# Kernel optimization log

Hardware: AMD Instinct MI355X
Metric: run time of the kernel (lower is better)

## Reference

```python
import jax, jax.numpy as jnp
import numpy as np

N = 4096
NUM_FEATURES = 1870
HIDDEN = 256
EMBED = 16
ALPHA = 0.2
NEG_BIG = -9e15
EPS = 1e-12


def setup_inputs() -> dict:
    key = jax.random.key(0)
    ks = jax.random.split(key, 9)
    x = jax.random.normal(ks[0], (N, NUM_FEATURES), dtype=jnp.float32)
    # sparse-ish binary adjacency mask (avg degree ~ 41) with self loops
    adj = (jax.random.uniform(ks[1], (N, N)) < 0.01).astype(jnp.float32)
    adj = jnp.maximum(adj, jnp.eye(N, dtype=jnp.float32))
    M = jax.random.uniform(ks[2], (N, N), dtype=jnp.float32)
    s1 = 1.0 / np.sqrt(NUM_FEATURES)
    s2 = 1.0 / np.sqrt(HIDDEN)
    W1 = jax.random.normal(ks[3], (NUM_FEATURES, HIDDEN), dtype=jnp.float32) * s1
    a_self1 = jax.random.normal(ks[4], (HIDDEN, 1), dtype=jnp.float32) * s2
    a_neighs1 = jax.random.normal(ks[5], (HIDDEN, 1), dtype=jnp.float32) * s2
    W2 = jax.random.normal(ks[6], (HIDDEN, EMBED), dtype=jnp.float32) * s2
    a_self2 = jax.random.normal(ks[7], (EMBED, 1), dtype=jnp.float32) / np.sqrt(EMBED)
    a_neighs2 = jax.random.normal(ks[8], (EMBED, 1), dtype=jnp.float32) / np.sqrt(EMBED)
    return {"x": x, "adj": adj, "M": M, "W1": W1, "a_self1": a_self1,
            "a_neighs1": a_neighs1, "W2": W2, "a_self2": a_self2, "a_neighs2": a_neighs2}


def gat_layer(x, adj, M, W, a_self, a_neighs, alpha):
    h = x @ W                                  # [N, out]
    f_self = h @ a_self                        # [N, 1]
    f_neigh = h @ a_neighs                     # [N, 1]
    e = jax.nn.leaky_relu((f_self + f_neigh.T) * M, negative_slope=alpha)  # [N, N]
    e = jnp.where(adj > 0, e, NEG_BIG)
    att = jax.nn.softmax(e, axis=1)            # row-stochastic over neighbors
    return jax.nn.elu(att @ h)                 # [N, out]


def reference(x, adj, M, W1, a_self1, a_neighs1, W2, a_self2, a_neighs2):
    h = gat_layer(x, adj, M, W1, a_self1, a_neighs1, ALPHA)
    h = gat_layer(h, adj, M, W2, a_self2, a_neighs2, ALPHA)
    # F.normalize(h, p=2, dim=1): divide by max(norm, eps)
    norm = jnp.maximum(jnp.linalg.norm(h, axis=1, keepdims=True), EPS)
    z = h / norm                               # [N, EMBED]
    A_pred = jax.nn.sigmoid(z @ z.T)           # [N, N]
    return (A_pred, z)
```

## Files before the change

kernel.cpp:

```cpp
#include <hip/hip_runtime.h>
#include <math.h>

#define NN 4096
#define NFEAT 1870
#define KPAD 1920
#define HID 256
#define EMB 16
#define MAXDEG 128

typedef __attribute__((ext_vector_type(8))) _Float16 f16x8;
typedef __attribute__((ext_vector_type(4))) float f32x4;

__device__ __forceinline__ ushort f2h(float f) {
    _Float16 h = (_Float16)f;
    return __builtin_bit_cast(ushort, h);
}

__global__ __launch_bounds__(256) void xcv_kernel(
    const float* __restrict__ x, ushort* __restrict__ xf)
{
    const int idx = blockIdx.x * 256 + threadIdx.x;
    const int row = idx / 240;
    const int c0 = (idx % 240) * 8;
    float v[8];
    if (c0 + 8 <= NFEAT) {
#pragma unroll
        for (int j = 0; j < 4; ++j) {
            float2 t = *(const float2*)&x[(size_t)row * NFEAT + c0 + j * 2];
            v[j * 2] = t.x; v[j * 2 + 1] = t.y;
        }
    } else {
#pragma unroll
        for (int j = 0; j < 8; ++j)
            v[j] = (c0 + j < NFEAT) ? x[(size_t)row * NFEAT + c0 + j] : 0.f;
    }
    ushort u[8];
#pragma unroll
    for (int j = 0; j < 8; ++j) u[j] = f2h(v[j]);
    *(int4*)&xf[(size_t)row * KPAD + c0] = *(int4*)u;
}

__global__ __launch_bounds__(256) void conv_w1t_kernel(
    const float* __restrict__ W1, ushort* __restrict__ Wh)
{
    __shared__ float t[64][65];
    const int tid = threadIdx.x;
    const int k0 = blockIdx.x * 64, n0 = blockIdx.y * 64;
    const int kk = tid >> 2, c4 = (tid & 3) * 16;
#pragma unroll
    for (int j = 0; j < 4; ++j) {
        int k = k0 + kk;
        float4 v = make_float4(0.f, 0.f, 0.f, 0.f);
        if (k < NFEAT) v = *(const float4*)&W1[(size_t)k * HID + n0 + c4 + j * 4];
        t[kk][c4 + j * 4 + 0] = v.x; t[kk][c4 + j * 4 + 1] = v.y;
        t[kk][c4 + j * 4 + 2] = v.z; t[kk][c4 + j * 4 + 3] = v.w;
    }
    __syncthreads();
    const int on = tid >> 2, ok4 = (tid & 3) * 16;
#pragma unroll
    for (int j = 0; j < 4; ++j) {
        ushort hh[4];
#pragma unroll
        for (int i = 0; i < 4; ++i)
            hh[i] = f2h(t[ok4 + j * 4 + i][on]);
        size_t o = (size_t)(n0 + on) * KPAD + k0 + ok4 + j * 4;
        *(ushort4*)&Wh[o] = *(ushort4*)hh;
    }
}

__global__ __launch_bounds__(256) void gemm_xw1(
    const ushort* __restrict__ Ag,
    const ushort* __restrict__ Bg,
    float* __restrict__ Cpart)
{
    __shared__ ushort Ah[128 * 64];
    __shared__ ushort Bh[64 * 64];
    const int tid = threadIdx.x;
    const int lane = tid & 63;
    const int w = tid >> 6;
    const int wr = w >> 1, wc = w & 1;
    const int row0 = blockIdx.x * 128;
    const int col0 = blockIdx.y * 64;
    const int kbeg = blockIdx.z * 512;
    const int kend = min(KPAD, kbeg + 512);
    const int nsteps = (kend - kbeg) >> 6;

    const int fr = lane & 15, fs = lane >> 4;

    const int a_row = tid >> 1;
    const int a_sk0 = (tid & 1) * 4;
    const int b_row = tid >> 2;
    const int b_sk0 = (tid & 3) * 2;

    const size_t a_gbase = (size_t)(row0 + a_row) * KPAD;
    const size_t b_gbase = (size_t)(col0 + b_row) * KPAD;

    int4 ra[4], rb[2];
#define LOADAB(K0)                                                        \
    {                                                                     \
        _Pragma("unroll")                                                 \
        for (int i = 0; i < 4; ++i)                                       \
            ra[i] = *(const int4*)&Ag[a_gbase + (K0) + (a_sk0 + i) * 8];  \
        _Pragma("unroll")                                                 \
        for (int i = 0; i < 2; ++i)                                       \
            rb[i] = *(const int4*)&Bg[b_gbase + (K0) + (b_sk0 + i) * 8];  \
    }

    LOADAB(kbeg);
    f32x4 acc[4][2] = {};

    for (int ks = 0; ks < nsteps; ++ks) {
        __syncthreads();
#pragma unroll
        for (int i = 0; i < 4; ++i)
            *(int4*)&Ah[(a_row * 8 + ((a_sk0 + i) ^ (a_row & 7))) * 8] = ra[i];
#pragma unroll
        for (int i = 0; i < 2; ++i)
            *(int4*)&Bh[(b_row * 8 + ((b_sk0 + i) ^ (b_row & 7))) * 8] = rb[i];
        __syncthreads();
        if (ks + 1 < nsteps) LOADAB(kbeg + (ks + 1) * 64);

        f16x8 af[4][2], bf[2][2];
#pragma unroll
        for (int m = 0; m < 4; ++m) {
            int r = wr * 64 + m * 16 + fr;
#pragma unroll
            for (int kf = 0; kf < 2; ++kf) {
                int sk = kf * 4 + fs;
                af[m][kf] = *(const f16x8*)&Ah[(r * 8 + (sk ^ (r & 7))) * 8];
            }
        }
#pragma unroll
        for (int n = 0; n < 2; ++n) {
            int r = wc * 32 + n * 16 + fr;
#pragma unroll
            for (int kf = 0; kf < 2; ++kf) {
                int sk = kf * 4 + fs;
                bf[n][kf] = *(const f16x8*)&Bh[(r * 8 + (sk ^ (r & 7))) * 8];
            }
        }
#pragma unroll
        for (int m = 0; m < 4; ++m)
#pragma unroll
            for (int n = 0; n < 2; ++n)
#pragma unroll
                for (int kf = 0; kf < 2; ++kf)
                    acc[m][n] = __builtin_amdgcn_mfma_f32_16x16x32_f16(
                        af[m][kf], bf[n][kf], acc[m][n], 0, 0, 0);
    }
    float* Cp = Cpart + (size_t)blockIdx.z * NN * HID;
#pragma unroll
    for (int m = 0; m < 4; ++m)
#pragma unroll
        for (int n = 0; n < 2; ++n)
#pragma unroll
            for (int r = 0; r < 4; ++r) {
                int row = row0 + wr * 64 + m * 16 + fs * 4 + r;
                int col = col0 + wc * 32 + n * 16 + fr;
                Cp[(size_t)row * HID + col] = acc[m][n][r];
            }
}

__global__ __launch_bounds__(256) void reduce_h1f_kernel(
    const float* __restrict__ part, float* __restrict__ h1,
    const float* __restrict__ a_s, const float* __restrict__ a_n,
    float* __restrict__ fs, float* __restrict__ fn)
{
    const int tid = threadIdx.x, wv = tid >> 6, lane = tid & 63;
    const int row = blockIdx.x * 4 + wv;
    const int d0 = lane * 4;
    const size_t o = (size_t)row * HID + d0;
    float4 s = *(const float4*)&part[o];
#pragma unroll
    for (int ch = 1; ch < 4; ++ch) {
        float4 p = *(const float4*)&part[(size_t)ch * NN * HID + o];
        s.x += p.x; s.y += p.y; s.z += p.z; s.w += p.w;
    }
    *(float4*)&h1[o] = s;
    float4 as4 = *(const float4*)&a_s[d0];
    float4 an4 = *(const float4*)&a_n[d0];
    float ps = s.x * as4.x + s.y * as4.y + s.z * as4.z + s.w * as4.w;
    float pn = s.x * an4.x + s.y * an4.y + s.z * an4.z + s.w * an4.w;
#pragma unroll
    for (int off = 32; off > 0; off >>= 1) {
        ps += __shfl_down(ps, off, 64);
        pn += __shfl_down(pn, off, 64);
    }
    if (lane == 0) { fs[row] = ps; fn[row] = pn; }
}

__global__ __launch_bounds__(256) void extract_kernel(
    const float* __restrict__ adj, const float* __restrict__ Mmat,
    int* __restrict__ nnz, int* __restrict__ gidx, float* __restrict__ Mg)
{
    __shared__ int sidx[4][MAXDEG];
    const int tid = threadIdx.x;
    const int wv = tid >> 6, lane = tid & 63;
    const int row = blockIdx.x * 4 + wv;

    int base = 0;
#pragma unroll 4
    for (int t = 0; t < 16; ++t) {
        int j0 = t * 256 + lane * 4;
        float4 a = *(const float4*)&adj[(size_t)row * NN + j0];
        float av[4] = {a.x, a.y, a.z, a.w};
#pragma unroll
        for (int c = 0; c < 4; ++c) {
            unsigned long long mb = __ballot(av[c] > 0.f);
            if (av[c] > 0.f) {
                int pos = base + (int)__popcll(mb & ((1ull << lane) - 1ull));
                if (pos < MAXDEG) sidx[wv][pos] = j0 + c;
            }
            base += (int)__popcll(mb);
        }
    }
    const int cnt = min(base, MAXDEG);
    if (lane == 0) nnz[row] = cnt;
    for (int s = lane; s < cnt; s += 64) {
        int j = sidx[wv][s];
        gidx[(size_t)row * MAXDEG + s] = j;
        Mg[(size_t)row * MAXDEG + s] = Mmat[(size_t)row * NN + j];
    }
}

__global__ __launch_bounds__(256) void spmm1_kernel(
    const int* __restrict__ nnz, const int* __restrict__ gidx,
    const float* __restrict__ Mg,
    const float* __restrict__ fs, const float* __restrict__ fn,
    const float* __restrict__ h1, float* __restrict__ g1)
{
    __shared__ float p_s[MAXDEG];
    __shared__ int j_s[MAXDEG];
    __shared__ float wred[4], wsum[4];
    const int row = blockIdx.x;
    const int tid = threadIdx.x;
    const int lane = tid & 63, wv = tid >> 6;
    const int cnt = nnz[row];
    const float fsi = fs[row];

    float lmax = -3.0e38f;
    for (int s = tid; s < cnt; s += 256) {
        int j = gidx[(size_t)row * MAXDEG + s];
        j_s[s] = j;
        float e = (fsi + fn[j]) * Mg[(size_t)row * MAXDEG + s];
        e = (e > 0.f) ? e : 0.2f * e;
        p_s[s] = e;
        lmax = fmaxf(lmax, e);
    }
#pragma unroll
    for (int off = 32; off > 0; off >>= 1)
        lmax = fmaxf(lmax, __shfl_down(lmax, off, 64));
    if (lane == 0) wred[wv] = lmax;
    __syncthreads();
    const float m = fmaxf(fmaxf(wred[0], wred[1]), fmaxf(wred[2], wred[3]));

    float lsum = 0.f;
    for (int s = tid; s < cnt; s += 256) {
        float p = __expf(p_s[s] - m);
        p_s[s] = p;
        lsum += p;
    }
#pragma unroll
    for (int off = 32; off > 0; off >>= 1)
        lsum += __shfl_down(lsum, off, 64);
    if (lane == 0) wsum[wv] = lsum;
    __syncthreads();
    const float inv = 1.f / (wsum[0] + wsum[1] + wsum[2] + wsum[3]);

    float acc = 0.f;
#pragma unroll 4
    for (int s = 0; s < cnt; ++s)
        acc += p_s[s] * h1[(size_t)j_s[s] * HID + tid];
    float v = acc * inv;
    v = (v > 0.f) ? v : (__expf(v) - 1.f);
    g1[(size_t)row * HID + tid] = v;
}

__global__ __launch_bounds__(256) void gemm_h2_kernel(
    const float* __restrict__ g1, const float* __restrict__ W2,
    const float* __restrict__ a_s2, const float* __restrict__ a_n2,
    float* __restrict__ h2, float* __restrict__ fs2, float* __restrict__ fn2)
{
    __shared__ float Ws[256][16];
    __shared__ float Gs[16][257];
    const int tid = threadIdx.x;
    const int row0 = blockIdx.x * 16;
#pragma unroll
    for (int i = 0; i < 16; ++i) {
        int idx = tid + i * 256;
        Ws[idx >> 4][idx & 15] = W2[idx];
    }
#pragma unroll
    for (int i = 0; i < 16; ++i) {
        int idx = tid + i * 256;
        Gs[idx >> 8][idx & 255] = g1[(size_t)(row0 + (idx >> 8)) * HID + (idx & 255)];
    }
    __syncthreads();
    const int r = tid >> 4, c = tid & 15;
    float acc = 0.f;
#pragma unroll 8
    for (int k = 0; k < 256; ++k)
        acc += Gs[r][k] * Ws[k][c];
    h2[(size_t)(row0 + r) * EMB + c] = acc;

    float ps = acc * a_s2[c];
    float pn = acc * a_n2[c];
#pragma unroll
    for (int off = 1; off < 16; off <<= 1) {
        ps += __shfl_xor(ps, off, 64);
        pn += __shfl_xor(pn, off, 64);
    }
    if (c == 0) { fs2[row0 + r] = ps; fn2[row0 + r] = pn; }
}

__global__ __launch_bounds__(256) void spmm2_kernel(
    const int* __restrict__ nnz, const int* __restrict__ gidx,
    const float* __restrict__ Mg,
    const float* __restrict__ fs, const float* __restrict__ fn,
    const float* __restrict__ h2, float* __restrict__ z)
{
    __shared__ float p_s[4][MAXDEG];
    __shared__ int j_s[4][MAXDEG];
    const int tid = threadIdx.x;
    const int wv = tid >> 6, lane = tid & 63;
    const int row = blockIdx.x * 4 + wv;
    const int cnt = nnz[row];
    const float fsi = fs[row];

    float lmax = -3.0e38f;
    for (int s = lane; s < cnt; s += 64) {
        int j = gidx[(size_t)row * MAXDEG + s];
        j_s[wv][s] = j;
        float e = (fsi + fn[j]) * Mg[(size_t)row * MAXDEG + s];
        e = (e > 0.f) ? e : 0.2f * e;
        p_s[wv][s] = e;
        lmax = fmaxf(lmax, e);
    }
#pragma unroll
    for (int off = 1; off < 64; off <<= 1)
        lmax = fmaxf(lmax, __shfl_xor(lmax, off, 64));

    float lsum = 0.f;
    for (int s = lane; s < cnt; s += 64) {
        float p = __expf(p_s[wv][s] - lmax);
        p_s[wv][s] = p;
        lsum += p;
    }
#pragma unroll
    for (int off = 1; off < 64; off <<= 1)
        lsum += __shfl_xor(lsum, off, 64);
    const float inv = 1.f / lsum;

    const int s0 = lane >> 4, d = lane & 15;
    float acc = 0.f;
    for (int s = s0; s < cnt; s += 4)
        acc += p_s[wv][s] * h2[(size_t)j_s[wv][s] * EMB + d];
    acc += __shfl_xor(acc, 16, 64);
    acc += __shfl_xor(acc, 32, 64);

    float v = acc * inv;
    v = (v > 0.f) ? v : (__expf(v) - 1.f);
    float ss = v * v;
#pragma unroll
    for (int off = 1; off < 16; off <<= 1)
        ss += __shfl_xor(ss, off, 64);
    float zn = v / fmaxf(sqrtf(ss), 1e-12f);
    if (lane < 16) z[(size_t)row * EMB + lane] = zn;
}

__global__ __launch_bounds__(256) void apred_kernel(
    const float* __restrict__ z, float* __restrict__ out)
{
    __shared__ float zr[64][20];
    __shared__ float zc[64][20];
    const int tid = threadIdx.x;
    const int r0 = blockIdx.y * 64, c0 = blockIdx.x * 64;
#pragma unroll
    for (int i = 0; i < 4; ++i) {
        int idx = tid + i * 256;
        int rr = idx >> 4, d = idx & 15;
        zr[rr][d] = z[(size_t)(r0 + rr) * EMB + d];
        zc[rr][d] = z[(size_t)(c0 + rr) * EMB + d];
    }
    __syncthreads();
    const int tx = tid & 15, ty = tid >> 4;
    float rb[4][16], cb[4][16];
#pragma unroll
    for (int i = 0; i < 4; ++i)
#pragma unroll
        for (int d = 0; d < 16; ++d) {
            rb[i][d] = zr[ty * 4 + i][d];
            cb[i][d] = zc[tx * 4 + i][d];
        }
#pragma unroll
    for (int i = 0; i < 4; ++i) {
        float4 o;
        float v[4];
#pragma unroll
        for (int j = 0; j < 4; ++j) {
            float s = 0.f;
#pragma unroll
            for (int d = 0; d < 16; ++d) s += rb[i][d] * cb[j][d];
            v[j] = 1.f / (1.f + __expf(-s));
        }
        o.x = v[0]; o.y = v[1]; o.z = v[2]; o.w = v[3];
        *reinterpret_cast<float4*>(
            &out[(size_t)(r0 + ty * 4 + i) * NN + c0 + tx * 4]) = o;
    }
}

extern "C" void kernel_launch(void* const* d_in, const int* in_sizes, int n_in,
                              void* d_out, int out_size, void* d_ws, size_t ws_size,
                              hipStream_t stream)
{
    const float* x    = (const float*)d_in[0];
    const float* adj  = (const float*)d_in[1];
    const float* Mm   = (const float*)d_in[2];
    const float* W1   = (const float*)d_in[3];
    const float* a_s1 = (const float*)d_in[4];
    const float* a_n1 = (const float*)d_in[5];
    const float* W2   = (const float*)d_in[6];
    const float* a_s2 = (const float*)d_in[7];
    const float* a_n2 = (const float*)d_in[8];

    float* out = (float*)d_out;
    float* z   = out + (size_t)NN * NN;

    char* w = (char*)d_ws;
    float* part  = (float*)w;  w += (size_t)4 * NN * HID * 4;
    float* h1    = (float*)w;  w += (size_t)NN * HID * 4;
    float* g1    = (float*)w;  w += (size_t)NN * HID * 4;
    ushort* xf16 = (ushort*)w; w += (size_t)NN * KPAD * 2;
    ushort* W1Th = (ushort*)w; w += (size_t)HID * KPAD * 2;
    float* h2    = (float*)w;  w += (size_t)NN * EMB * 4;
    int*   nnzp  = (int*)w;    w += NN * 4;
    int*   gidx  = (int*)w;    w += (size_t)NN * MAXDEG * 4;
    float* Mg    = (float*)w;  w += (size_t)NN * MAXDEG * 4;
    float* fs1   = (float*)w;  w += NN * 4;
    float* fn1   = (float*)w;  w += NN * 4;
    float* fs2   = (float*)w;  w += NN * 4;
    float* fn2   = (float*)w;  w += NN * 4;

    xcv_kernel<<<NN * 240 / 256, 256, 0, stream>>>(x, xf16);
    conv_w1t_kernel<<<dim3(30, 4), 256, 0, stream>>>(W1, W1Th);
    extract_kernel<<<NN / 4, 256, 0, stream>>>(adj, Mm, nnzp, gidx, Mg);

    gemm_xw1<<<dim3(32, 4, 4), 256, 0, stream>>>(xf16, W1Th, part);
    reduce_h1f_kernel<<<NN / 4, 256, 0, stream>>>(part, h1, a_s1, a_n1, fs1, fn1);
    spmm1_kernel<<<NN, 256, 0, stream>>>(nnzp, gidx, Mg, fs1, fn1, h1, g1);

    gemm_h2_kernel<<<256, 256, 0, stream>>>(g1, W2, a_s2, a_n2, h2, fs2, fn2);
    spmm2_kernel<<<NN / 4, 256, 0, stream>>>(nnzp, gidx, Mg, fs2, fn2, h2, z);

    apred_kernel<<<dim3(64, 64), 256, 0, stream>>>(z, out);
}
```

Before: 117.7 us.

## Fuse prep kernels, use LDS-free split-K GEMM, stage partials in output buffer

Merges the x conversion, W1 transpose and adjacency extraction into one launch with block-range dispatch. The X·W1 GEMM drops LDS staging and barriers: each wave loads MFMA fragments straight from global memory. K is padded to 2048 and split 8 ways into 256-wide chunks on a 1D grid. Split-K partials now go into the A_pred output region, which apred_kernel overwrites later, so the workspace is smaller. The risks are more uncoalesced global fragment loads and double the partial-sum traffic in the reduce step.

Result: faster. 109.4 us (-7.1%).

```diff
diff --git a/kernel.cpp b/kernel.cpp
--- a/kernel.cpp
+++ b/kernel.cpp
@@ -3,7 +3,9 @@
 
 #define NN 4096
 #define NFEAT 1870
-#define KPAD 1920
+#define KPAD 2048
+#define KSPLIT 8
+#define KCHUNK 256
 #define HID 256
 #define EMB 16
 #define MAXDEG 128
@@ -16,147 +18,133 @@
     return __builtin_bit_cast(ushort, h);
 }
 
-__global__ __launch_bounds__(256) void xcv_kernel(
-    const float* __restrict__ x, ushort* __restrict__ xf)
-{
-    const int idx = blockIdx.x * 256 + threadIdx.x;
-    const int row = idx / 240;
-    const int c0 = (idx % 240) * 8;
-    float v[8];
-    if (c0 + 8 <= NFEAT) {
+__global__ __launch_bounds__(256) void prep_kernel(
+    const float* __restrict__ x, ushort* __restrict__ xf,
+    const float* __restrict__ W1, ushort* __restrict__ Wh,
+    const float* __restrict__ adj, const float* __restrict__ Mmat,
+    int* __restrict__ nnz, int* __restrict__ gidx, float* __restrict__ Mg)
+{
+    const int b = blockIdx.x;
+    const int tid = threadIdx.x;
+    if (b < NN) {
+        const int row = b;
+        const int c0 = tid * 8;
+        float v[8];
+        if (c0 + 8 <= NFEAT) {
+#pragma unroll
+            for (int j = 0; j < 4; ++j) {
+                float2 t = *(const float2*)&x[(size_t)row * NFEAT + c0 + j * 2];
+                v[j * 2] = t.x; v[j * 2 + 1] = t.y;
+            }
+        } else {
+#pragma unroll
+            for (int j = 0; j < 8; ++j)
+                v[j] = (c0 + j < NFEAT) ? x[(size_t)row * NFEAT + c0 + j] : 0.f;
+        }
+        ushort u[8];
+#pragma unroll
+        for (int j = 0; j < 8; ++j) u[j] = f2h(v[j]);
+        *(int4*)&xf[(size_t)row * KPAD + c0] = *(int4*)u;
+    } else if (b < NN + 128) {
+        __shared__ float t[64][65];
+        const int bb = b - NN;
+        const int k0 = (bb & 31) * 64, n0 = (bb >> 5) * 64;
+        const int kk = tid >> 2, c4 = (tid & 3) * 16;
 #pragma unroll
         for (int j = 0; j < 4; ++j) {
-            float2 t = *(const float2*)&x[(size_t)row * NFEAT + c0 + j * 2];
-            v[j * 2] = t.x; v[j * 2 + 1] = t.y;
+            int k = k0 + kk;
+            float4 v = make_float4(0.f, 0.f, 0.f, 0.f);
+            if (k < NFEAT) v = *(const float4*)&W1[(size_t)k * HID + n0 + c4 + j * 4];
+            t[kk][c4 + j * 4 + 0] = v.x; t[kk][c4 + j * 4 + 1] = v.y;
+            t[kk][c4 + j * 4 + 2] = v.z; t[kk][c4 + j * 4 + 3] = v.w;
+        }
+        __syncthreads();
+        const int on = tid >> 2, ok4 = (tid & 3) * 16;
+#pragma unroll
+        for (int j = 0; j < 4; ++j) {
+            ushort hh[4];
+#pragma unroll
+            for (int i = 0; i < 4; ++i)
+                hh[i] = f2h(t[ok4 + j * 4 + i][on]);
+            size_t o = (size_t)(n0 + on) * KPAD + k0 + ok4 + j * 4;
+            *(ushort4*)&Wh[o] = *(ushort4*)hh;
         }
     } else {
-#pragma unroll
-        for (int j = 0; j < 8; ++j)
-            v[j] = (c0 + j < NFEAT) ? x[(size_t)row * NFEAT + c0 + j] : 0.f;
-    }
-    ushort u[8];
-#pragma unroll
-    for (int j = 0; j < 8; ++j) u[j] = f2h(v[j]);
-    *(int4*)&xf[(size_t)row * KPAD + c0] = *(int4*)u;
-}
-
-__global__ __launch_bounds__(256) void conv_w1t_kernel(
-    const float* __restrict__ W1, ushort* __restrict__ Wh)
-{
-    __shared__ float t[64][65];
-    const int tid = threadIdx.x;
-    const int k0 = blockIdx.x * 64, n0 = blockIdx.y * 64;
-    const int kk = tid >> 2, c4 = (tid & 3) * 16;
-#pragma unroll
-    for (int j = 0; j < 4; ++j) {
-        int k = k0 + kk;
-        float4 v = make_float4(0.f, 0.f, 0.f, 0.f);
-        if (k < NFEAT) v = *(const float4*)&W1[(size_t)k * HID + n0 + c4 + j * 4];
-        t[kk][c4 + j * 4 + 0] = v.x; t[kk][c4 + j * 4 + 1] = v.y;
-        t[kk][c4 + j * 4 + 2] = v.z; t[kk][c4 + j * 4 + 3] = v.w;
-    }
-    __syncthreads();
-    const int on = tid >> 2, ok4 = (tid & 3) * 16;
-#pragma unroll
-    for (int j = 0; j < 4; ++j) {
-        ushort hh[4];
-#pragma unroll
-        for (int i = 0; i < 4; ++i)
-            hh[i] = f2h(t[ok4 + j * 4 + i][on]);
-        size_t o = (size_t)(n0 + on) * KPAD + k0 + ok4 + j * 4;
-        *(ushort4*)&Wh[o] = *(ushort4*)hh;
-    }
-}
-
-__global__ __launch_bounds__(256) void gemm_xw1(
+        __shared__ int sidx[4][MAXDEG];
+        const int bb = b - NN - 128;
+        const int wv = tid >> 6, lane = tid & 63;
+        const int row = bb * 4 + wv;
+        int base = 0;
+#pragma unroll 4
+        for (int t4 = 0; t4 < 16; ++t4) {
+            int j0 = t4 * 256 + lane * 4;
+            float4 a = *(const float4*)&adj[(size_t)row * NN + j0];
+            float av[4] = {a.x, a.y, a.z, a.w};
+#pragma unroll
+            for (int c = 0; c < 4; ++c) {
+                unsigned long long mb = __ballot(av[c] > 0.f);
+                if (av[c] > 0.f) {
+                    int pos = base + (int)__popcll(mb & ((1ull << lane) - 1ull));
+                    if (pos < MAXDEG) sidx[wv][pos] = j0 + c;
+                }
+                base += (int)__popcll(mb);
+            }
+        }
+        const int cnt = min(base, MAXDEG);
+        if (lane == 0) nnz[row] = cnt;
+        for (int s = lane; s < cnt; s += 64) {
+            int j = sidx[wv][s];
+            gidx[(size_t)row * MAXDEG + s] = j;
+            Mg[(size_t)row * MAXDEG + s] = Mmat[(size_t)row * NN + j];
+        }
+    }
+}
+
+__global__ __launch_bounds__(256, 4) void gemm_xw1(
     const ushort* __restrict__ Ag,
     const ushort* __restrict__ Bg,
     float* __restrict__ Cpart)
 {
-    __shared__ ushort Ah[128 * 64];
-    __shared__ ushort Bh[64 * 64];
     const int tid = threadIdx.x;
     const int lane = tid & 63;
-    const int w = tid >> 6;
-    const int wr = w >> 1, wc = w & 1;
-    const int row0 = blockIdx.x * 128;
-    const int col0 = blockIdx.y * 64;
-    const int kbeg = blockIdx.z * 512;
-    const int kend = min(KPAD, kbeg + 512);
-    const int nsteps = (kend - kbeg) >> 6;
+    const int cgrp = tid >> 6;
+    const int mgrp = blockIdx.x >> 3;
+    const int z    = blockIdx.x & 7;
+    const int row0 = mgrp * 32;
+    const int col0 = cgrp * 64;
+    const int kbeg = z * KCHUNK;
 
     const int fr = lane & 15, fs = lane >> 4;
 
-    const int a_row = tid >> 1;
-    const int a_sk0 = (tid & 1) * 4;
-    const int b_row = tid >> 2;
-    const int b_sk0 = (tid & 3) * 2;
-
-    const size_t a_gbase = (size_t)(row0 + a_row) * KPAD;
-    const size_t b_gbase = (size_t)(col0 + b_row) * KPAD;
-
-    int4 ra[4], rb[2];
-#define LOADAB(K0)                                                        \
-    {                                                                     \
-        _Pragma("unroll")                                                 \
-        for (int i = 0; i < 4; ++i)                                       \
-            ra[i] = *(const int4*)&Ag[a_gbase + (K0) + (a_sk0 + i) * 8];  \
-        _Pragma("unroll")                                                 \
-        for (int i = 0; i < 2; ++i)                                       \
-            rb[i] = *(const int4*)&Bg[b_gbase + (K0) + (b_sk0 + i) * 8];  \
-    }
-
-    LOADAB(kbeg);
-    f32x4 acc[4][2] = {};
-
-    for (int ks = 0; ks < nsteps; ++ks) {
-        __syncthreads();
-#pragma unroll
-        for (int i = 0; i < 4; ++i)
-            *(int4*)&Ah[(a_row * 8 + ((a_sk0 + i) ^ (a_row & 7))) * 8] = ra[i];
-#pragma unroll
-        for (int i = 0; i < 2; ++i)
-            *(int4*)&Bh[(b_row * 8 + ((b_sk0 + i) ^ (b_row & 7))) * 8] = rb[i];
-        __syncthreads();
-        if (ks + 1 < nsteps) LOADAB(kbeg + (ks + 1) * 64);
-
-        f16x8 af[4][2], bf[2][2];
-#pragma unroll
-        for (int m = 0; m < 4; ++m) {
-            int r = wr * 64 + m * 16 + fr;
-#pragma unroll
-            for (int kf = 0; kf < 2; ++kf) {
-                int sk = kf * 4 + fs;
-                af[m][kf] = *(const f16x8*)&Ah[(r * 8 + (sk ^ (r & 7))) * 8];
-            }
-        }
-#pragma unroll
-        for (int n = 0; n < 2; ++n) {
-            int r = wc * 32 + n * 16 + fr;
-#pragma unroll
-            for (int kf = 0; kf < 2; ++kf) {
-                int sk = kf * 4 + fs;
-                bf[n][kf] = *(const f16x8*)&Bh[(r * 8 + (sk ^ (r & 7))) * 8];
-            }
-        }
-#pragma unroll
-        for (int m = 0; m < 4; ++m)
-#pragma unroll
-            for (int n = 0; n < 2; ++n)
-#pragma unroll
-                for (int kf = 0; kf < 2; ++kf)
-                    acc[m][n] = __builtin_amdgcn_mfma_f32_16x16x32_f16(
-                        af[m][kf], bf[n][kf], acc[m][n], 0, 0, 0);
-    }
-    float* Cp = Cpart + (size_t)blockIdx.z * NN * HID;
-#pragma unroll
-    for (int m = 0; m < 4; ++m)
-#pragma unroll
-        for (int n = 0; n < 2; ++n)
+    const ushort* Abase = Ag + (size_t)(row0 + fr) * KPAD + kbeg + fs * 8;
+    const ushort* Bbase = Bg + (size_t)(col0 + fr) * KPAD + kbeg + fs * 8;
+
+    f32x4 acc[2][4] = {};
+#pragma unroll
+    for (int sk = 0; sk < 8; ++sk) {
+        f16x8 a[2], b[4];
+#pragma unroll
+        for (int m = 0; m < 2; ++m)
+            a[m] = *(const f16x8*)&Abase[(size_t)m * 16 * KPAD + sk * 32];
+#pragma unroll
+        for (int n = 0; n < 4; ++n)
+            b[n] = *(const f16x8*)&Bbase[(size_t)n * 16 * KPAD + sk * 32];
+#pragma unroll
+        for (int m = 0; m < 2; ++m)
+#pragma unroll
+            for (int n = 0; n < 4; ++n)
+                acc[m][n] = __builtin_amdgcn_mfma_f32_16x16x32_f16(
+                    a[m], b[n], acc[m][n], 0, 0, 0);
+    }
+    float* Cp = Cpart + (size_t)z * NN * HID;
+#pragma unroll
+    for (int m = 0; m < 2; ++m)
+#pragma unroll
+        for (int n = 0; n < 4; ++n)
 #pragma unroll
             for (int r = 0; r < 4; ++r) {
-                int row = row0 + wr * 64 + m * 16 + fs * 4 + r;
-                int col = col0 + wc * 32 + n * 16 + fr;
+                int row = row0 + m * 16 + fs * 4 + r;
+                int col = col0 + n * 16 + fr;
                 Cp[(size_t)row * HID + col] = acc[m][n][r];
             }
 }
@@ -172,7 +160,7 @@
     const size_t o = (size_t)row * HID + d0;
     float4 s = *(const float4*)&part[o];
 #pragma unroll
-    for (int ch = 1; ch < 4; ++ch) {
+    for (int ch = 1; ch < KSPLIT; ++ch) {
         float4 p = *(const float4*)&part[(size_t)ch * NN * HID + o];
         s.x += p.x; s.y += p.y; s.z += p.z; s.w += p.w;
     }
@@ -187,40 +175,6 @@
         pn += __shfl_down(pn, off, 64);
     }
     if (lane == 0) { fs[row] = ps; fn[row] = pn; }
-}
-
-__global__ __launch_bounds__(256) void extract_kernel(
-    const float* __restrict__ adj, const float* __restrict__ Mmat,
-    int* __restrict__ nnz, int* __restrict__ gidx, float* __restrict__ Mg)
-{
-    __shared__ int sidx[4][MAXDEG];
-    const int tid = threadIdx.x;
-    const int wv = tid >> 6, lane = tid & 63;
-    const int row = blockIdx.x * 4 + wv;
-
-    int base = 0;
-#pragma unroll 4
-    for (int t = 0; t < 16; ++t) {
-        int j0 = t * 256 + lane * 4;
-        float4 a = *(const float4*)&adj[(size_t)row * NN + j0];
-        float av[4] = {a.x, a.y, a.z, a.w};
-#pragma unroll
-        for (int c = 0; c < 4; ++c) {
-            unsigned long long mb = __ballot(av[c] > 0.f);
-            if (av[c] > 0.f) {
-                int pos = base + (int)__popcll(mb & ((1ull << lane) - 1ull));
-                if (pos < MAXDEG) sidx[wv][pos] = j0 + c;
-            }
-            base += (int)__popcll(mb);
-        }
-    }
-    const int cnt = min(base, MAXDEG);
-    if (lane == 0) nnz[row] = cnt;
-    for (int s = lane; s < cnt; s += 64) {
-        int j = sidx[wv][s];
-        gidx[(size_t)row * MAXDEG + s] = j;
-        Mg[(size_t)row * MAXDEG + s] = Mmat[(size_t)row * NN + j];
-    }
 }
 
 __global__ __launch_bounds__(256) void spmm1_kernel(
@@ -425,9 +379,9 @@
 
     float* out = (float*)d_out;
     float* z   = out + (size_t)NN * NN;
+    float* part = out;
 
     char* w = (char*)d_ws;
-    float* part  = (float*)w;  w += (size_t)4 * NN * HID * 4;
     float* h1    = (float*)w;  w += (size_t)NN * HID * 4;
     float* g1    = (float*)w;  w += (size_t)NN * HID * 4;
     ushort* xf16 = (ushort*)w; w += (size_t)NN * KPAD * 2;
@@ -441,11 +395,10 @@
     float* fs2   = (float*)w;  w += NN * 4;
     float* fn2   = (float*)w;  w += NN * 4;
 
-    xcv_kernel<<<NN * 240 / 256, 256, 0, stream>>>(x, xf16);
-    conv_w1t_kernel<<<dim3(30, 4), 256, 0, stream>>>(W1, W1Th);
-    extract_kernel<<<NN / 4, 256, 0, stream>>>(adj, Mm, nnzp, gidx, Mg);
-
-    gemm_xw1<<<dim3(32, 4, 4), 256, 0, stream>>>(xf16, W1Th, part);
+    prep_kernel<<<NN + 128 + NN / 4, 256, 0, stream>>>(
+        x, xf16, W1, W1Th, adj, Mm, nnzp, gidx, Mg);
+
+    gemm_xw1<<<(NN / 32) * KSPLIT, 256, 0, stream>>>(xf16, W1Th, part);
     reduce_h1f_kernel<<<NN / 4, 256, 0, stream>>>(part, h1, a_s1, a_n1, fs1, fn1);
     spmm1_kernel<<<NN, 256, 0, stream>>>(nnzp, gidx, Mg, fs1, fn1, h1, g1);
 
```
